# Kernel optimization log

Measured on AMD Instinct MI355X. Metric: run time of the kernel, lower is better.

Reference implementation:

```python
import jax, jax.numpy as jnp
import numpy as np

DN = ('NCHW', 'HWIO', 'NCHW')  # NCHW data, HWIO kernels


def conv3x3(x, k, b=None):
    # 'same'-padded 3x3 conv, stride 1, NCHW layout
    y = jax.lax.conv_general_dilated(x, k, (1, 1), 'SAME', dimension_numbers=DN)
    if b is not None:
        y = y + b[None, :, None, None]
    return y


def setup_inputs() -> dict:
    B, T, C, H, W = 4, 4, 256, 30, 40
    CA = 256  # nb_filters_att (== nb_filters_out == nb_filters_in per SAM)
    key = jax.random.key(0)
    ks = jax.random.split(key, 10)
    s = 0.05  # small init scale so gates don't saturate
    x = jax.random.normal(ks[0], (B, T, C, H, W), dtype=jnp.float32)
    # attention convs
    Wa = jax.random.normal(ks[1], (3, 3, C, CA), dtype=jnp.float32) * s
    ba = jnp.zeros((CA,), dtype=jnp.float32)
    Ua = jax.random.normal(ks[2], (3, 3, C, CA), dtype=jnp.float32) * s
    bua = jnp.zeros((CA,), dtype=jnp.float32)
    # V_a has attentive_init='zero' in the original; random here for a nontrivial baseline
    Va = jax.random.normal(ks[3], (3, 3, CA, 1), dtype=jnp.float32) * s
    # gate convs: stack i,f,c,o along output channels (same math as 4 separate 3x3 convs)
    Wx = jax.random.normal(ks[4], (3, 3, C, 4 * C), dtype=jnp.float32) * s
    bx = jnp.zeros((4 * C,), dtype=jnp.float32)
    Uh = jax.random.normal(ks[5], (3, 3, C, 4 * C), dtype=jnp.float32) * s
    bh = jnp.zeros((4 * C,), dtype=jnp.float32)
    return {"x": x, "Wa": Wa, "ba": ba, "Ua": Ua, "bua": bua, "Va": Va,
            "Wx": Wx, "bx": bx, "Uh": Uh, "bh": bh}


def reference(x, Wa, ba, Ua, bua, Va, Wx, bx, Uh, bh):
    B, T, C, H, W = x.shape
    # initial h and c: sum over the time axis (K.sum(x, axis=1))
    h0 = jnp.sum(x, axis=1)
    c0 = h0

    def step(carry, xt):
        h, c = carry
        # conv-based spatial attention
        e = conv3x3(jnp.tanh(conv3x3(h, Wa, ba) + conv3x3(xt, Ua, bua)), Va)  # [B,1,H,W]
        a = jax.nn.softmax(e.reshape(B, -1), axis=-1).reshape(B, 1, H, W)
        x_tilde = xt * a  # broadcast over channels
        # fused gate convs: i | f | c | o along channel axis
        g = conv3x3(x_tilde, Wx, bx) + conv3x3(h, Uh, bh)  # [B,4C,H,W]
        gi, gf, gc, go = jnp.split(g, 4, axis=1)
        i = jax.nn.sigmoid(gi)
        f = jax.nn.sigmoid(gf)
        o = jax.nn.sigmoid(go)
        c_new = f * c + i * jnp.tanh(gc)
        h_new = o * jnp.tanh(c_new)
        return (h_new, c_new), None

    (h_last, _), _ = jax.lax.scan(step, (h0, c0), jnp.swapaxes(x, 0, 1))
    return h_last  # [B, C_out, H, W], the last RNN output
```

## Files before the change

kernel.cpp:

```cpp
#include <hip/hip_runtime.h>
#include <math.h>

#define BB 4
#define TT 4
#define CC 256
#define HH 30
#define WW 40
#define HWS (HH*WW)
#define CHW (CC*HWS)
#define CHW4 (CHW/4)
#define NCG 32
#define PXS (NCG*HWS*8)
#define PL 168

typedef __attribute__((ext_vector_type(8))) _Float16 half8;
typedef __attribute__((ext_vector_type(4))) float f32x4;

__global__ void pack_x16(const float* __restrict__ x, _Float16* __restrict__ x16) {
    int id = blockIdx.x * 256 + threadIdx.x;
    if (id >= BB * TT * NCG * HWS) return;
    int p = id % HWS;
    int cig = (id / HWS) % NCG;
    int bt = id / (HWS * NCG);
    const float* src = x + ((size_t)bt * CC + cig * 8) * HWS + p;
    half8 hv;
#pragma unroll
    for (int j = 0; j < 8; ++j) hv[j] = (_Float16)src[(size_t)j * HWS];
    *(half8*)&x16[(size_t)id * 8] = hv;
}

__global__ void init_hc(const float* __restrict__ x, _Float16* __restrict__ h16,
                        float* __restrict__ c) {
    int id = blockIdx.x * 256 + threadIdx.x;
    if (id >= BB * NCG * HWS) return;
    int p = id % HWS;
    int cig = (id / HWS) % NCG;
    int b = id / (HWS * NCG);
    float s[8];
#pragma unroll
    for (int j = 0; j < 8; ++j) s[j] = 0.f;
#pragma unroll
    for (int t = 0; t < TT; ++t) {
        const float* src = x + (((size_t)b * TT + t) * CC + cig * 8) * HWS + p;
#pragma unroll
        for (int j = 0; j < 8; ++j) s[j] += src[(size_t)j * HWS];
    }
    half8 hv;
    float* cp = c + ((size_t)b * CC + cig * 8) * HWS + p;
#pragma unroll
    for (int j = 0; j < 8; ++j) { cp[(size_t)j * HWS] = s[j]; hv[j] = (_Float16)s[j]; }
    *(half8*)&h16[(size_t)id * 8] = hv;
}

__global__ void xtilde_kernel(const float* __restrict__ xt, const float* __restrict__ a,
                              _Float16* __restrict__ xt16) {
    int id = blockIdx.x * 256 + threadIdx.x;
    if (id >= BB * NCG * HWS) return;
    int p = id % HWS;
    int cig = (id / HWS) % NCG;
    int b = id / (HWS * NCG);
    float sc = a[(size_t)b * HWS + p];
    const float* src = xt + ((size_t)b * TT * CC + cig * 8) * HWS + p;
    half8 hv;
#pragma unroll
    for (int j = 0; j < 8; ++j) hv[j] = (_Float16)(src[(size_t)j * HWS] * sc);
    *(half8*)&xt16[(size_t)id * 8] = hv;
}

__global__ void pack_weights(const float* __restrict__ W1,
                             const float* __restrict__ W2,
                             _Float16* __restrict__ wt, int Cout) {
    int idx = blockIdx.x * 256 + threadIdx.x;
    if (idx >= 4608 * Cout) return;
    int k = idx / Cout;
    int n = idx - k * Cout;
    float v = (k < 2304) ? W1[(size_t)k * Cout + n]
                         : W2[(size_t)(k - 2304) * Cout + n];
    wt[((size_t)(k >> 3) * Cout + n) * 8 + (k & 7)] = (_Float16)v;
}

template<int NW, int NZ, int NY, int ZT>
__global__ __launch_bounds__(256, 2) void conv_mfma(
    const _Float16* __restrict__ in0, long bs0,
    const _Float16* __restrict__ in1, long bs1,
    const _Float16* __restrict__ wt,
    const float* __restrict__ b1, const float* __restrict__ b2,
    float* __restrict__ out, int Cout)
{
    constexpr int NK = 8 / NZ;
    constexpr int SLICES = NY * ZT;
    constexpr int PERX = SLICES / 8;
    __shared__ alignas(16) _Float16 s_a[2][4 * PL * 8];

    const int tid = threadIdx.x;
    const int l = tid & 63, wv = tid >> 6;
    const int q = l >> 4, r = l & 15;

    const int lin = blockIdx.x;
    const int xcd = lin & 7;
    const int idx = lin >> 3;
    const int sl = xcd * PERX + idx / 60;
    const int mb = idx % 60;
    const int zz = sl / NY;
    const int yy = sl - zz * NY;

    const int b = mb / 15;
    const int pix0 = (mb % 15) * 80;
    const int y0 = (mb % 15) * 2;
    const int n0 = yy * (4 * NW * 16) + wv * (NW * 16);
    const int src = zz / NZ;
    const int ci_start = (zz % NZ) * (CC / NZ);
    const int kgb0 = src * 288 + (ci_start >> 3);

    const _Float16* inp = src ? (in1 + (size_t)b * bs1) : (in0 + (size_t)b * bs0);

    bool iv[3], pv[3];
    const _Float16* pj[3];
    int ldsoff[3];
#pragma unroll
    for (int j = 0; j < 3; ++j) {
        int item = tid + j * 256;
        iv[j] = item < 672;
        int it = iv[j] ? item : 0;
        int cig = it / 168;
        int pix = it - cig * 168;
        int row = pix / 42;
        int px = pix - row * 42;
        int xx = px - 1, yy2 = y0 + row - 1;
        pv[j] = iv[j] && xx >= 0 && xx < WW && yy2 >= 0 && yy2 < HH;
        pj[j] = inp + ((size_t)((ci_start >> 3) + cig) * HWS + yy2 * WW + xx) * 8;
        ldsoff[j] = (cig * PL + pix) * 8;
    }

    f32x4 acc[5][NW];
#pragma unroll
    for (int nt = 0; nt < NW; ++nt) {
        int co = n0 + nt * 16 + r;
        float bias = (zz == 0) ? (b1[co] + b2[co]) : 0.f;
        f32x4 bv = {bias, bias, bias, bias};
#pragma unroll
        for (int mt = 0; mt < 5; ++mt) acc[mt][nt] = bv;
    }

    int hbase[5];
#pragma unroll
    for (int mt = 0; mt < 5; ++mt) {
        int p = mt * 16 + r;
        int ry = p / 40;
        int rx = p - ry * 40;
        hbase[mt] = ry * 42 + rx;
    }

    half8 sr[3];
    auto stage_issue = [&](int kk) {
#pragma unroll
        for (int j = 0; j < 3; ++j) if (pv[j])
            sr[j] = *(const half8*)(pj[j] + (size_t)kk * (4 * HWS * 8));
    };
    auto stage_write = [&](int kk) {
#pragma unroll
        for (int j = 0; j < 3; ++j) if (iv[j]) {
            half8 hv = {0, 0, 0, 0, 0, 0, 0, 0};
            if (pv[j]) hv = sr[j];
            *(half8*)&s_a[kk & 1][ldsoff[j]] = hv;
        }
    };

    const half8* wp = (const half8*)wt;
    half8 w0[NW], w1[NW], w2[NW], w3[NW];

#define WLOAD(SLOT, TAP) do {                                              \
    const int kg_ = kgb0 + k * 4 + (TAP) * 32 + q;                         \
    _Pragma("unroll")                                                      \
    for (int nt = 0; nt < NW; ++nt)                                        \
        SLOT[nt] = wp[(size_t)kg_ * Cout + n0 + nt * 16 + r];              \
} while (0)

#define CTAP(SLOT, TAP) do {                                               \
    constexpr int dy_ = (TAP) / 3, dx_ = (TAP) % 3;                        \
    _Pragma("unroll")                                                      \
    for (int mt = 0; mt < 5; ++mt) {                                       \
        half8 af = *(const half8*)&s_a[k & 1]                              \
            [(q * PL + hbase[mt] + dy_ * 42 + dx_) * 8];                   \
        _Pragma("unroll")                                                  \
        for (int nt = 0; nt < NW; ++nt)                                    \
            acc[mt][nt] = __builtin_amdgcn_mfma_f32_16x16x32_f16(          \
                af, SLOT[nt], acc[mt][nt], 0, 0, 0);                       \
    }                                                                      \
} while (0)

    stage_issue(0);
    stage_write(0);

#pragma unroll
    for (int k = 0; k < NK; ++k) {
        WLOAD(w0, 0); WLOAD(w1, 1); WLOAD(w2, 2);
        if (k + 1 < NK) stage_issue(k + 1);
        __syncthreads();
        __builtin_amdgcn_s_setprio(1);
        WLOAD(w3, 3); CTAP(w0, 0);
        WLOAD(w0, 4); CTAP(w1, 1);
        WLOAD(w1, 5); CTAP(w2, 2);
        WLOAD(w2, 6); CTAP(w3, 3);
        WLOAD(w3, 7); CTAP(w0, 4);
        WLOAD(w0, 8); CTAP(w1, 5);
        CTAP(w2, 6);
        CTAP(w3, 7);
        CTAP(w0, 8);
        __builtin_amdgcn_s_setprio(0);
        if (k + 1 < NK) stage_write(k + 1);
    }
#undef WLOAD
#undef CTAP

    out += (size_t)zz * BB * Cout * HWS;
#pragma unroll
    for (int mt = 0; mt < 5; ++mt) {
#pragma unroll
        for (int nt = 0; nt < NW; ++nt) {
            int co = n0 + nt * 16 + r;
            int p = pix0 + mt * 16 + q * 4;
            *(f32x4*)&out[((size_t)b * Cout + co) * HWS + p] = acc[mt][nt];
        }
    }
}

__global__ void add_tanh4(const float* __restrict__ a0,
                          float* __restrict__ o, int n4) {
    int id = blockIdx.x * 256 + threadIdx.x;
    if (id >= n4) return;
    const f32x4* av = (const f32x4*)a0;
    f32x4 s = av[id] + av[id + (size_t)n4] + av[id + 2 * (size_t)n4]
            + av[id + 3 * (size_t)n4];
    f32x4 rr;
#pragma unroll
    for (int j = 0; j < 4; ++j) rr[j] = tanhf(s[j]);
    ((f32x4*)o)[id] = rr;
}

__global__ __launch_bounds__(256) void att_e_part(
    const float* __restrict__ att, const float* __restrict__ Va,
    float* __restrict__ part)
{
    __shared__ float red[4][64];
    const int lane = threadIdx.x & 63, wv = threadIdx.x >> 6;
    const int p = blockIdx.x * 64 + lane;
    const int b = blockIdx.y, ch = blockIdx.z;
    const bool valid = (p < HWS);
    const int pc = valid ? p : 0;
    const int y = pc / WW, x = pc - (pc / WW) * WW;

    float acc = 0.f;
    if (valid) {
        const int ca0 = ch * 32 + wv * 8;
#pragma unroll
        for (int j = 0; j < 8; ++j) {
            const int ca = ca0 + j;
            const float* base = att + ((size_t)b * CC + ca) * HWS;
            const float* va = Va + ca;
#pragma unroll
            for (int dy = 0; dy < 3; ++dy) {
                int yy = y + dy - 1;
                if (yy < 0 || yy >= HH) continue;
#pragma unroll
                for (int dx = 0; dx < 3; ++dx) {
                    int xx = x + dx - 1;
                    if (xx < 0 || xx >= WW) continue;
                    acc = fmaf(base[yy * WW + xx], va[(dy * 3 + dx) * CC], acc);
                }
            }
        }
    }
    red[wv][lane] = acc;
    __syncthreads();
    if (wv == 0 && valid)
        part[((size_t)b * 8 + ch) * HWS + p] =
            red[0][lane] + red[1][lane] + red[2][lane] + red[3][lane];
}

__global__ __launch_bounds__(256) void softmax_kernel(
    const float* __restrict__ part, float* __restrict__ a)
{
    __shared__ float se[HWS];
    __shared__ float red[256];
    int b = blockIdx.x;
    int tid = threadIdx.x;

    for (int i = tid; i < HWS; i += 256) {
        float s = 0.f;
#pragma unroll
        for (int ch = 0; ch < 8; ++ch)
            s += part[((size_t)b * 8 + ch) * HWS + i];
        se[i] = s;
    }
    __syncthreads();

    float m = -1e30f;
    for (int i = tid; i < HWS; i += 256) m = fmaxf(m, se[i]);
    red[tid] = m;
    __syncthreads();
    for (int s = 128; s > 0; s >>= 1) {
        if (tid < s) red[tid] = fmaxf(red[tid], red[tid + s]);
        __syncthreads();
    }
    m = red[0];
    __syncthreads();

    float sum = 0.f;
    for (int i = tid; i < HWS; i += 256) {
        float v = expf(se[i] - m);
        se[i] = v;
        sum += v;
    }
    red[tid] = sum;
    __syncthreads();
    for (int s = 128; s > 0; s >>= 1) {
        if (tid < s) red[tid] += red[tid + s];
        __syncthreads();
    }
    float inv = 1.f / red[0];
    for (int i = tid; i < HWS; i += 256)
        a[(size_t)b * HWS + i] = se[i] * inv;
}

__global__ void gate_update(const float* __restrict__ g0, const float* __restrict__ g1,
                            float* __restrict__ c, _Float16* __restrict__ h16,
                            float* __restrict__ h32) {
    int id = blockIdx.x * 256 + threadIdx.x;
    if (id >= BB * NCG * HWS) return;
    int p = id % HWS;
    int cig = (id / HWS) % NCG;
    int b = id / (HWS * NCG);
    const int ci0 = cig * 8;
    half8 hv;
#pragma unroll
    for (int j = 0; j < 8; ++j) {
        size_t base = ((size_t)b * 4 * CC + ci0 + j) * HWS + p;
        float gi = g0[base] + g1[base];
        float gf = g0[base + (size_t)CHW] + g1[base + (size_t)CHW];
        float gc = g0[base + 2 * (size_t)CHW] + g1[base + 2 * (size_t)CHW];
        float go = g0[base + 3 * (size_t)CHW] + g1[base + 3 * (size_t)CHW];
        float i_ = 1.f / (1.f + expf(-gi));
        float f_ = 1.f / (1.f + expf(-gf));
        float o_ = 1.f / (1.f + expf(-go));
        size_t cix = ((size_t)b * CC + ci0 + j) * HWS + p;
        float cn = f_ * c[cix] + i_ * tanhf(gc);
        c[cix] = cn;
        float hn = o_ * tanhf(cn);
        hv[j] = (_Float16)hn;
        if (h32) h32[cix] = hn;
    }
    *(half8*)&h16[(size_t)id * 8] = hv;
}

extern "C" void kernel_launch(void* const* d_in, const int* in_sizes, int n_in,
                              void* d_out, int out_size, void* d_ws, size_t ws_size,
                              hipStream_t stream) {
    const float* x   = (const float*)d_in[0];
    const float* Wa  = (const float*)d_in[1];
    const float* ba  = (const float*)d_in[2];
    const float* Ua  = (const float*)d_in[3];
    const float* bua = (const float*)d_in[4];
    const float* Va  = (const float*)d_in[5];
    const float* Wx  = (const float*)d_in[6];
    const float* bx  = (const float*)d_in[7];
    const float* Uh  = (const float*)d_in[8];
    const float* bh  = (const float*)d_in[9];
    float* out = (float*)d_out;

    char* wsb = (char*)d_ws;
    const size_t NCHW = (size_t)BB * CHW;
    _Float16* wtg  = (_Float16*)wsb;              wsb += (size_t)4608 * 1024 * 2;
    _Float16* wta  = (_Float16*)wsb;              wsb += (size_t)4608 * 256 * 2;
    _Float16* x16  = (_Float16*)wsb;              wsb += (size_t)BB * TT * PXS * 2;
    _Float16* h16  = (_Float16*)wsb;              wsb += (size_t)BB * PXS * 2;
    _Float16* xt16 = (_Float16*)wsb;              wsb += (size_t)BB * PXS * 2;
    float* cb   = (float*)wsb;                    wsb += NCHW * 4;
    float* g01  = (float*)wsb;                    wsb += 8 * NCHW * 4;
    float* att  = (float*)wsb;                    wsb += NCHW * 4;
    float* part = (float*)wsb;                    wsb += (size_t)BB * 8 * HWS * 4;
    float* a    = (float*)wsb;
    float* att01 = g01;

    pack_weights<<<dim3((4608 * 1024 + 255) / 256), dim3(256), 0, stream>>>(
        Wx, Uh, wtg, 1024);
    pack_weights<<<dim3((4608 * 256 + 255) / 256), dim3(256), 0, stream>>>(
        Wa, Ua, wta, 256);
    pack_x16<<<dim3((BB * TT * NCG * HWS + 255) / 256), dim3(256), 0, stream>>>(
        x, x16);

    const int nblk = BB * NCG * HWS;
    init_hc<<<dim3((nblk + 255) / 256), dim3(256), 0, stream>>>(x, h16, cb);

    const int n4 = (int)(NCHW / 4);

    for (int t = 0; t < TT; ++t) {
        conv_mfma<2, 2, 2, 4><<<dim3(480), dim3(256), 0, stream>>>(
            h16, (long)PXS, x16 + (size_t)t * PXS, (long)TT * PXS,
            wta, ba, bua, att01, 256);
        add_tanh4<<<dim3((n4 + 255) / 256), dim3(256), 0, stream>>>(
            att01, att, n4);

        att_e_part<<<dim3(19, BB, 8), dim3(256), 0, stream>>>(att, Va, part);
        softmax_kernel<<<dim3(BB), dim3(256), 0, stream>>>(part, a);

        xtilde_kernel<<<dim3((nblk + 255) / 256), dim3(256), 0, stream>>>(
            x + (size_t)t * CHW, a, xt16);

        conv_mfma<4, 1, 4, 2><<<dim3(480), dim3(256), 0, stream>>>(
            xt16, (long)PXS, h16, (long)PXS, wtg, bx, bh, g01, 1024);

        gate_update<<<dim3((nblk + 255) / 256), dim3(256), 0, stream>>>(
            g01, g01 + 4 * NCHW, cb, h16, (t == TT - 1) ? out : nullptr);
    }
}
```

Measured before the change: 561.1 us.

## Process two batch images per conv block to reuse weight fragments

The MFMA conv kernel now handles two batch elements per block, each with its own LDS input tile, so every loaded weight fragment feeds twice as many MFMAs. The gate conv switches from NW=4 to NW=2 with twice as many output-channel slices, which keeps the accumulator count at 80 and the grid at 480 blocks. The attention conv keeps NW=2, so its grid halves to 240 blocks. The change doubles LDS usage and staging registers, and the attention conv's accumulators double, which may cut occupancy and leave fewer blocks to fill the CUs.

```diff
diff --git a/kernel.cpp b/kernel.cpp
--- a/kernel.cpp
+++ b/kernel.cpp
@@ -11,7 +11,7 @@
 #define CHW4 (CHW/4)
 #define NCG 32
 #define PXS (NCG*HWS*8)
-#define PL 168
+#define TS (4*168*8)
 
 typedef __attribute__((ext_vector_type(8))) _Float16 half8;
 typedef __attribute__((ext_vector_type(4))) float f32x4;
@@ -90,7 +90,8 @@
     constexpr int NK = 8 / NZ;
     constexpr int SLICES = NY * ZT;
     constexpr int PERX = SLICES / 8;
-    __shared__ alignas(16) _Float16 s_a[2][4 * PL * 8];
+    constexpr int MU = 30;
+    __shared__ alignas(16) _Float16 s_a[2][2 * TS];
 
     const int tid = threadIdx.x;
     const int l = tid & 63, wv = tid >> 6;
@@ -99,67 +100,76 @@
     const int lin = blockIdx.x;
     const int xcd = lin & 7;
     const int idx = lin >> 3;
-    const int sl = xcd * PERX + idx / 60;
-    const int mb = idx % 60;
+    const int sl = xcd * PERX + idx / MU;
+    const int mu = idx % MU;
     const int zz = sl / NY;
     const int yy = sl - zz * NY;
 
-    const int b = mb / 15;
-    const int pix0 = (mb % 15) * 80;
-    const int y0 = (mb % 15) * 2;
+    const int pairb = mu / 15;
+    const int rt = mu % 15;
+    const int b0 = pairb * 2;
+    const int pix0 = rt * 80;
+    const int y0 = rt * 2;
     const int n0 = yy * (4 * NW * 16) + wv * (NW * 16);
     const int src = zz / NZ;
     const int ci_start = (zz % NZ) * (CC / NZ);
     const int kgb0 = src * 288 + (ci_start >> 3);
 
-    const _Float16* inp = src ? (in1 + (size_t)b * bs1) : (in0 + (size_t)b * bs0);
-
-    bool iv[3], pv[3];
-    const _Float16* pj[3];
-    int ldsoff[3];
-#pragma unroll
-    for (int j = 0; j < 3; ++j) {
+    const _Float16* inp[2];
+#pragma unroll
+    for (int bb = 0; bb < 2; ++bb)
+        inp[bb] = (src ? (in1 + (size_t)(b0 + bb) * bs1)
+                       : (in0 + (size_t)(b0 + bb) * bs0))
+                  + (size_t)(ci_start >> 3) * HWS * 8;
+
+    bool iv[6], pv[6];
+    const _Float16* pj[6];
+    int ldsoff[6];
+#pragma unroll
+    for (int j = 0; j < 6; ++j) {
         int item = tid + j * 256;
-        iv[j] = item < 672;
+        iv[j] = item < 1344;
         int it = iv[j] ? item : 0;
-        int cig = it / 168;
-        int pix = it - cig * 168;
+        int bsel = it / 672;
+        int it2 = it - bsel * 672;
+        int cig = it2 / 168;
+        int pix = it2 - cig * 168;
         int row = pix / 42;
         int px = pix - row * 42;
         int xx = px - 1, yy2 = y0 + row - 1;
         pv[j] = iv[j] && xx >= 0 && xx < WW && yy2 >= 0 && yy2 < HH;
-        pj[j] = inp + ((size_t)((ci_start >> 3) + cig) * HWS + yy2 * WW + xx) * 8;
-        ldsoff[j] = (cig * PL + pix) * 8;
-    }
-
-    f32x4 acc[5][NW];
+        pj[j] = inp[bsel] + ((size_t)cig * HWS + yy2 * WW + xx) * 8;
+        ldsoff[j] = bsel * TS + (cig * 168 + pix) * 8;
+    }
+
+    f32x4 acc[10][NW];
 #pragma unroll
     for (int nt = 0; nt < NW; ++nt) {
         int co = n0 + nt * 16 + r;
         float bias = (zz == 0) ? (b1[co] + b2[co]) : 0.f;
         f32x4 bv = {bias, bias, bias, bias};
 #pragma unroll
-        for (int mt = 0; mt < 5; ++mt) acc[mt][nt] = bv;
+        for (int mt = 0; mt < 10; ++mt) acc[mt][nt] = bv;
     }
 
     int hbase[5];
 #pragma unroll
-    for (int mt = 0; mt < 5; ++mt) {
-        int p = mt * 16 + r;
+    for (int m5 = 0; m5 < 5; ++m5) {
+        int p = m5 * 16 + r;
         int ry = p / 40;
         int rx = p - ry * 40;
-        hbase[mt] = ry * 42 + rx;
-    }
-
-    half8 sr[3];
+        hbase[m5] = ry * 42 + rx;
+    }
+
+    half8 sr[6];
     auto stage_issue = [&](int kk) {
 #pragma unroll
-        for (int j = 0; j < 3; ++j) if (pv[j])
+        for (int j = 0; j < 6; ++j) if (pv[j])
             sr[j] = *(const half8*)(pj[j] + (size_t)kk * (4 * HWS * 8));
     };
     auto stage_write = [&](int kk) {
 #pragma unroll
-        for (int j = 0; j < 3; ++j) if (iv[j]) {
+        for (int j = 0; j < 6; ++j) if (iv[j]) {
             half8 hv = {0, 0, 0, 0, 0, 0, 0, 0};
             if (pv[j]) hv = sr[j];
             *(half8*)&s_a[kk & 1][ldsoff[j]] = hv;
@@ -179,9 +189,10 @@
 #define CTAP(SLOT, TAP) do {                                               \
     constexpr int dy_ = (TAP) / 3, dx_ = (TAP) % 3;                        \
     _Pragma("unroll")                                                      \
-    for (int mt = 0; mt < 5; ++mt) {                                       \
+    for (int mt = 0; mt < 10; ++mt) {                                      \
         half8 af = *(const half8*)&s_a[k & 1]                              \
-            [(q * PL + hbase[mt] + dy_ * 42 + dx_) * 8];                   \
+            [(mt < 5 ? 0 : TS) +                                           \
+             (q * 168 + hbase[mt % 5] + dy_ * 42 + dx_) * 8];              \
         _Pragma("unroll")                                                  \
         for (int nt = 0; nt < NW; ++nt)                                    \
             acc[mt][nt] = __builtin_amdgcn_mfma_f32_16x16x32_f16(          \
@@ -215,11 +226,12 @@
 
     out += (size_t)zz * BB * Cout * HWS;
 #pragma unroll
-    for (int mt = 0; mt < 5; ++mt) {
+    for (int mt = 0; mt < 10; ++mt) {
 #pragma unroll
         for (int nt = 0; nt < NW; ++nt) {
             int co = n0 + nt * 16 + r;
-            int p = pix0 + mt * 16 + q * 4;
+            int b = b0 + (mt < 5 ? 0 : 1);
+            int p = pix0 + (mt % 5) * 16 + q * 4;
             *(f32x4*)&out[((size_t)b * Cout + co) * HWS + p] = acc[mt][nt];
         }
     }
@@ -395,7 +407,7 @@
     const int n4 = (int)(NCHW / 4);
 
     for (int t = 0; t < TT; ++t) {
-        conv_mfma<2, 2, 2, 4><<<dim3(480), dim3(256), 0, stream>>>(
+        conv_mfma<2, 2, 2, 4><<<dim3(240), dim3(256), 0, stream>>>(
             h16, (long)PXS, x16 + (size_t)t * PXS, (long)TT * PXS,
             wta, ba, bua, att01, 256);
         add_tanh4<<<dim3((n4 + 255) / 256), dim3(256), 0, stream>>>(
@@ -407,7 +419,7 @@
         xtilde_kernel<<<dim3((nblk + 255) / 256), dim3(256), 0, stream>>>(
             x + (size_t)t * CHW, a, xt16);
 
-        conv_mfma<4, 1, 4, 2><<<dim3(480), dim3(256), 0, stream>>>(
+        conv_mfma<2, 1, 8, 2><<<dim3(480), dim3(256), 0, stream>>>(
             xt16, (long)PXS, h16, (long)PXS, wtg, bx, bh, g01, 1024);
 
         gate_update<<<dim3((nblk + 255) / 256), dim3(256), 0, stream>>>(
```

Measured after the change: 572.3 us. 2.0% more time.

## Switch conv kernels to 32x32x16 MFMA with larger pixel and channel tiles

Applied to the files above, without the earlier changes.

The implicit-GEMM conv moves from 16x16x32 to 32x32x16 MFMA. Each block now covers 160 pixels (4 image rows) and 32-wide output-channel groups, and the grid shrinks to 256 blocks with launch bounds of 1 block per CU. The attention conv uses a 4-way input-channel split, so the follow-up tanh kernel now sums 8 partial outputs. The aim is more reuse per LDS and weight load and fewer MFMA issues per FLOP. In exchange there are fewer resident waves per CU, padded rows past H=30, and extra partial-sum traffic for the attention path.

```diff
diff --git a/kernel.cpp b/kernel.cpp
--- a/kernel.cpp
+++ b/kernel.cpp
@@ -8,13 +8,13 @@
 #define WW 40
 #define HWS (HH*WW)
 #define CHW (CC*HWS)
-#define CHW4 (CHW/4)
 #define NCG 32
 #define PXS (NCG*HWS*8)
-#define PL 168
+#define PLANE 2016
 
 typedef __attribute__((ext_vector_type(8))) _Float16 half8;
 typedef __attribute__((ext_vector_type(4))) float f32x4;
+typedef __attribute__((ext_vector_type(16))) float f32x16;
 
 __global__ void pack_x16(const float* __restrict__ x, _Float16* __restrict__ x16) {
     int id = blockIdx.x * 256 + threadIdx.x;
@@ -80,7 +80,7 @@
 }
 
 template<int NW, int NZ, int NY, int ZT>
-__global__ __launch_bounds__(256, 2) void conv_mfma(
+__global__ __launch_bounds__(256, 1) void conv_mfma(
     const _Float16* __restrict__ in0, long bs0,
     const _Float16* __restrict__ in1, long bs1,
     const _Float16* __restrict__ wt,
@@ -90,76 +90,81 @@
     constexpr int NK = 8 / NZ;
     constexpr int SLICES = NY * ZT;
     constexpr int PERX = SLICES / 8;
-    __shared__ alignas(16) _Float16 s_a[2][4 * PL * 8];
+    constexpr int MU = 32;
+    __shared__ alignas(16) _Float16 s_a[2][4 * PLANE];
 
     const int tid = threadIdx.x;
     const int l = tid & 63, wv = tid >> 6;
-    const int q = l >> 4, r = l & 15;
+    const int half = l >> 5;
+    const int lane_co = l & 31;
 
     const int lin = blockIdx.x;
     const int xcd = lin & 7;
     const int idx = lin >> 3;
-    const int sl = xcd * PERX + idx / 60;
-    const int mb = idx % 60;
+    const int sl = xcd * PERX + idx / MU;
+    const int mu = idx % MU;
     const int zz = sl / NY;
     const int yy = sl - zz * NY;
 
-    const int b = mb / 15;
-    const int pix0 = (mb % 15) * 80;
-    const int y0 = (mb % 15) * 2;
-    const int n0 = yy * (4 * NW * 16) + wv * (NW * 16);
+    const int b = mu >> 3;
+    const int rt = mu & 7;
+    const int pix0 = rt * 160;
+    const int y0 = rt * 4;
+    const int n0 = yy * (4 * NW * 32) + wv * (NW * 32);
     const int src = zz / NZ;
     const int ci_start = (zz % NZ) * (CC / NZ);
     const int kgb0 = src * 288 + (ci_start >> 3);
 
-    const _Float16* inp = src ? (in1 + (size_t)b * bs1) : (in0 + (size_t)b * bs0);
-
-    bool iv[3], pv[3];
-    const _Float16* pj[3];
-    int ldsoff[3];
-#pragma unroll
-    for (int j = 0; j < 3; ++j) {
+    const _Float16* inp = (src ? (in1 + (size_t)b * bs1) : (in0 + (size_t)b * bs0))
+                          + (size_t)(ci_start >> 3) * HWS * 8;
+
+    bool iv[4], pv[4];
+    const _Float16* pj[4];
+    int ldsoff[4];
+#pragma unroll
+    for (int j = 0; j < 4; ++j) {
         int item = tid + j * 256;
-        iv[j] = item < 672;
+        iv[j] = item < 1008;
         int it = iv[j] ? item : 0;
-        int cig = it / 168;
-        int pix = it - cig * 168;
+        int cig = it / 252;
+        int pix = it - cig * 252;
         int row = pix / 42;
         int px = pix - row * 42;
         int xx = px - 1, yy2 = y0 + row - 1;
         pv[j] = iv[j] && xx >= 0 && xx < WW && yy2 >= 0 && yy2 < HH;
-        pj[j] = inp + ((size_t)((ci_start >> 3) + cig) * HWS + yy2 * WW + xx) * 8;
-        ldsoff[j] = (cig * PL + pix) * 8;
-    }
-
-    f32x4 acc[5][NW];
+        pj[j] = inp + ((size_t)cig * HWS + yy2 * WW + xx) * 8;
+        ldsoff[j] = cig * PLANE + pix * 8;
+    }
+
+    f32x16 acc[5][NW];
 #pragma unroll
     for (int nt = 0; nt < NW; ++nt) {
-        int co = n0 + nt * 16 + r;
+        int co = n0 + nt * 32 + lane_co;
         float bias = (zz == 0) ? (b1[co] + b2[co]) : 0.f;
-        f32x4 bv = {bias, bias, bias, bias};
-#pragma unroll
-        for (int mt = 0; mt < 5; ++mt) acc[mt][nt] = bv;
-    }
-
-    int hbase[5];
-#pragma unroll
-    for (int mt = 0; mt < 5; ++mt) {
-        int p = mt * 16 + r;
+#pragma unroll
+        for (int f = 0; f < 5; ++f)
+#pragma unroll
+            for (int rg = 0; rg < 16; ++rg) acc[f][nt][rg] = bias;
+    }
+
+    int hb[5];
+#pragma unroll
+    for (int f = 0; f < 5; ++f) {
+        int p = f * 32 + lane_co;
         int ry = p / 40;
         int rx = p - ry * 40;
-        hbase[mt] = ry * 42 + rx;
-    }
-
-    half8 sr[3];
+        hb[f] = ry * 42 + rx;
+    }
+
+    half8 sr[4];
     auto stage_issue = [&](int kk) {
 #pragma unroll
-        for (int j = 0; j < 3; ++j) if (pv[j])
+        for (int j = 0; j < 4; ++j) if (pv[j])
             sr[j] = *(const half8*)(pj[j] + (size_t)kk * (4 * HWS * 8));
     };
     auto stage_write = [&](int kk) {
 #pragma unroll
-        for (int j = 0; j < 3; ++j) if (iv[j]) {
+        for (int j = 0; j < 4; ++j) if (iv[j]) {
             half8 hv = {0, 0, 0, 0, 0, 0, 0, 0};
             if (pv[j]) hv = sr[j];
             *(half8*)&s_a[kk & 1][ldsoff[j]] = hv;
@@ -167,25 +172,29 @@
     };
 
     const half8* wp = (const half8*)wt;
-    half8 w0[NW], w1[NW], w2[NW], w3[NW];
-
-#define WLOAD(SLOT, TAP) do {                                              \
-    const int kg_ = kgb0 + k * 4 + (TAP) * 32 + q;                         \
+    half8 wA[2][NW], wB[2][NW];
+
+#define WLOADX(S, TAP) do {                                                \
+    _Pragma("unroll")                                                      \
+    for (int ks = 0; ks < 2; ++ks)                                         \
     _Pragma("unroll")                                                      \
     for (int nt = 0; nt < NW; ++nt)                                        \
-        SLOT[nt] = wp[(size_t)kg_ * Cout + n0 + nt * 16 + r];              \
+        S[ks][nt] = wp[(size_t)(kgb0 + k * 4 + (TAP) * 32 + ks * 2 + half) \
+                       * Cout + n0 + nt * 32 + lane_co];                   \
 } while (0)
 
-#define CTAP(SLOT, TAP) do {                                               \
+#define CTAPX(S, TAP) do {                                                 \
     constexpr int dy_ = (TAP) / 3, dx_ = (TAP) % 3;                        \
     _Pragma("unroll")                                                      \
-    for (int mt = 0; mt < 5; ++mt) {                                       \
+    for (int f = 0; f < 5; ++f)                                            \
+    _Pragma("unroll")                                                      \
+    for (int ks = 0; ks < 2; ++ks) {                                       \
         half8 af = *(const half8*)&s_a[k & 1]                              \
-            [(q * PL + hbase[mt] + dy_ * 42 + dx_) * 8];                   \
+            [(ks * 2 + half) * PLANE + (hb[f] + dy_ * 42 + dx_) * 8];      \
         _Pragma("unroll")                                                  \
         for (int nt = 0; nt < NW; ++nt)                                    \
-            acc[mt][nt] = __builtin_amdgcn_mfma_f32_16x16x32_f16(          \
-                af, SLOT[nt], acc[mt][nt], 0, 0, 0);                       \
+            acc[f][nt] = __builtin_amdgcn_mfma_f32_32x32x16_f16(           \
+                af, S[ks][nt], acc[f][nt], 0, 0, 0);                       \
     }                                                                      \
 } while (0)
 
@@ -194,44 +203,53 @@
 
 #pragma unroll
     for (int k = 0; k < NK; ++k) {
-        WLOAD(w0, 0); WLOAD(w1, 1); WLOAD(w2, 2);
-        if (k + 1 < NK) stage_issue(k + 1);
+        WLOADX(wA, 0);
         __syncthreads();
         __builtin_amdgcn_s_setprio(1);
-        WLOAD(w3, 3); CTAP(w0, 0);
-        WLOAD(w0, 4); CTAP(w1, 1);
-        WLOAD(w1, 5); CTAP(w2, 2);
-        WLOAD(w2, 6); CTAP(w3, 3);
-        WLOAD(w3, 7); CTAP(w0, 4);
-        WLOAD(w0, 8); CTAP(w1, 5);
-        CTAP(w2, 6);
-        CTAP(w3, 7);
-        CTAP(w0, 8);
+        if (k + 1 < NK) stage_issue(k + 1);
+        WLOADX(wB, 1); CTAPX(wA, 0);
+        WLOADX(wA, 2); CTAPX(wB, 1);
+        WLOADX(wB, 3); CTAPX(wA, 2);
+        WLOADX(wA, 4); CTAPX(wB, 3);
+        WLOADX(wB, 5); CTAPX(wA, 4);
+        WLOADX(wA, 6); CTAPX(wB, 5);
+        WLOADX(wB, 7); CTAPX(wA, 6);
+        WLOADX(wA, 8); CTAPX(wB, 7);
+        CTAPX(wA, 8);
         __builtin_amdgcn_s_setprio(0);
         if (k + 1 < NK) stage_write(k + 1);
     }
-#undef WLOAD
-#undef CTAP
+#undef WLOADX
+#undef CTAPX
 
     out += (size_t)zz * BB * Cout * HWS;
 #pragma unroll
-    for (int mt = 0; mt < 5; ++mt) {
+    for (int f = 0; f < 5; ++f) {
 #pragma unroll
         for (int nt = 0; nt < NW; ++nt) {
-            int co = n0 + nt * 16 + r;
-            int p = pix0 + mt * 16 + q * 4;
-            *(f32x4*)&out[((size_t)b * Cout + co) * HWS + p] = acc[mt][nt];
+            int co = n0 + nt * 32 + lane_co;
+            float* op = out + ((size_t)b * Cout + co) * HWS;
+#pragma unroll
+            for (int rg = 0; rg < 4; ++rg) {
+                int px = pix0 + f * 32 + 8 * rg + 4 * half;
+                if (px < HWS) {
+                    f32x4 v = {acc[f][nt][4 * rg], acc[f][nt][4 * rg + 1],
+                               acc[f][nt][4 * rg + 2], acc[f][nt][4 * rg + 3]};
+                    *(f32x4*)&op[px] = v;
+                }
+            }
         }
     }
 }
 
-__global__ void add_tanh4(const float* __restrict__ a0,
+__global__ void add_tanh8(const float* __restrict__ a0,
                           float* __restrict__ o, int n4) {
     int id = blockIdx.x * 256 + threadIdx.x;
     if (id >= n4) return;
     const f32x4* av = (const f32x4*)a0;
-    f32x4 s = av[id] + av[id + (size_t)n4] + av[id + 2 * (size_t)n4]
-            + av[id + 3 * (size_t)n4];
+    f32x4 s = {0.f, 0.f, 0.f, 0.f};
+#pragma unroll
+    for (int z = 0; z < 8; ++z) s += av[id + (size_t)z * n4];
     f32x4 rr;
 #pragma unroll
     for (int j = 0; j < 4; ++j) rr[j] = tanhf(s[j]);
@@ -395,10 +413,10 @@
     const int n4 = (int)(NCHW / 4);
 
     for (int t = 0; t < TT; ++t) {
-        conv_mfma<2, 2, 2, 4><<<dim3(480), dim3(256), 0, stream>>>(
+        conv_mfma<2, 4, 1, 8><<<dim3(256), dim3(256), 0, stream>>>(
             h16, (long)PXS, x16 + (size_t)t * PXS, (long)TT * PXS,
             wta, ba, bua, att01, 256);
-        add_tanh4<<<dim3((n4 + 255) / 256), dim3(256), 0, stream>>>(
+        add_tanh8<<<dim3((n4 + 255) / 256), dim3(256), 0, stream>>>(
             att01, att, n4);
 
         att_e_part<<<dim3(19, BB, 8), dim3(256), 0, stream>>>(att, Va, part);
@@ -407,7 +425,7 @@
         xtilde_kernel<<<dim3((nblk + 255) / 256), dim3(256), 0, stream>>>(
             x + (size_t)t * CHW, a, xt16);
 
-        conv_mfma<4, 1, 4, 2><<<dim3(480), dim3(256), 0, stream>>>(
+        conv_mfma<2, 1, 4, 2><<<dim3(256), dim3(256), 0, stream>>>(
             xt16, (long)PXS, h16, (long)PXS, wtg, bx, bh, g01, 1024);
 
         gate_update<<<dim3((nblk + 255) / 256), dim3(256), 0, stream>>>(
```

Result: slower. 634.7 us (+13.1%).
